# Kernel optimization log

Hardware: AMD Instinct MI355X
Metric: run time of the kernel (lower is better)

## Reference

```python
import jax, jax.numpy as jnp
import numpy as np

N_NODES = 100000


def gcn_conv(x, edge_index, W, b):
    # PyG GCNConv: add self-loops, symmetric normalization, then scatter-add.
    n = x.shape[0]
    loops = jnp.arange(n, dtype=edge_index.dtype)
    src = jnp.concatenate([edge_index[0], loops])
    dst = jnp.concatenate([edge_index[1], loops])
    h = x @ W  # [N, F_out] -- transform before propagate (small GEMM)
    ones = jnp.ones(src.shape[0], dtype=x.dtype)
    deg = jax.ops.segment_sum(ones, dst, num_segments=n)  # in-degree incl. self-loop
    dinv = jnp.where(deg > 0, jax.lax.rsqrt(deg), 0.0)
    norm = dinv[src] * dinv[dst]  # [E+N]
    msg = h[src] * norm[:, None]  # gather + scale, [E+N, F_out]
    out = jax.ops.segment_sum(msg, dst, num_segments=n)  # scatter-add
    return out + b


def setup_inputs() -> dict:
    key = jax.random.key(0)
    k1, k2, k3, k4 = jax.random.split(key, 4)
    d = 128
    x = jax.random.normal(k1, (N_NODES, d), dtype=jnp.float32)
    edge_index = jax.random.randint(k2, (2, 1600000), 0, N_NODES, dtype=jnp.int64)
    scale = 1.0 / np.sqrt(d)
    W1 = jax.random.normal(k3, (d, d), dtype=jnp.float32) * scale
    b1 = jnp.zeros((d,), dtype=jnp.float32)
    W2 = jax.random.normal(k4, (d, d), dtype=jnp.float32) * scale
    b2 = jnp.zeros((d,), dtype=jnp.float32)
    return {"x": x, "edge_index": edge_index, "W1": W1, "b1": b1, "W2": W2, "b2": b2}


def reference(x, edge_index, W1, b1, W2, b2):
    # Layer 1: GCNConv -> relu -> dropout(eval: identity)
    h = jax.nn.relu(gcn_conv(x, edge_index, W1, b1))
    # Layer 2
    h = jax.nn.relu(gcn_conv(h, edge_index, W2, b2))
    return h
```

## Files before the change

### kernel.cpp

```cpp
#include <hip/hip_runtime.h>


#define NFEAT 128
#define BSH 7
#define MAXNB 1024
#define BCAP 4096
#define BPITCH 136

typedef __attribute__((ext_vector_type(8))) short s8v;
typedef __attribute__((ext_vector_type(4))) float f4v;

__device__ inline ushort f2bf(float f) {
    union { float f; uint u; } x; x.f = f;
    uint u = x.u;
    return (ushort)((u + 0x7fffu + ((u >> 16) & 1u)) >> 16);
}
__device__ inline float bf16lo(uint u) { union { uint u; float f; } x; x.u = u << 16; return x.f; }
__device__ inline float bf16hi(uint u) { union { uint u; float f; } x; x.u = u & 0xffff0000u; return x.f; }

__device__ inline void upadd(uint4 v, float* a) {
    a[0] += bf16lo(v.x); a[1] += bf16hi(v.x);
    a[2] += bf16lo(v.y); a[3] += bf16hi(v.y);
    a[4] += bf16lo(v.z); a[5] += bf16hi(v.z);
    a[6] += bf16lo(v.w); a[7] += bf16hi(v.w);
}

__global__ __launch_bounds__(256) void k_bscatter(const int* __restrict__ src,
                                                  const int* __restrict__ dst,
                                                  int* __restrict__ gcnt,
                                                  uint* __restrict__ ebuf,
                                                  int E, int NB, int CH) {
    __shared__ int h[MAXNB];
    int t = threadIdx.x;
    for (int i = t; i < NB; i += 256) h[i] = 0;
    __syncthreads();
    int e0 = blockIdx.x * CH;
    int e1 = min(e0 + CH, E);
    for (int e = e0 + t; e < e1; e += 256) atomicAdd(&h[dst[e] >> BSH], 1);
    __syncthreads();
    for (int i = t; i < NB; i += 256) {
        int c = h[i];
        h[i] = c ? (i * BCAP + atomicAdd(&gcnt[i], c)) : 0;
    }
    __syncthreads();
    for (int e = e0 + t; e < e1; e += 256) {
        int d = dst[e];
        int b = d >> BSH;
        int p = atomicAdd(&h[b], 1);
        if (p < (b + 1) * BCAP)
            ebuf[p] = ((uint)src[e] << BSH) | (uint)(d & ((1 << BSH) - 1));
    }
}

__global__ __launch_bounds__(256) void k_fill2(const uint* __restrict__ ebuf,
                                               const int* __restrict__ gcnt,
                                               int* __restrict__ row_ptr,
                                               float* __restrict__ dinv,
                                               int* __restrict__ col,
                                               int N, int E, int NB) {
    __shared__ int cnt[128];
    __shared__ int pre[128];
    __shared__ int sred[256];
    __shared__ int colL[BCAP];
    int b = blockIdx.x;
    int t = threadIdx.x;
    int part = 0;
    for (int j = t; j < b; j += 256) part += gcnt[j];
    sred[t] = part;
    __syncthreads();
    for (int off = 128; off >= 1; off >>= 1) {
        if (t < off) sred[t] += sred[t + off];
        __syncthreads();
    }
    int gb = sred[0];
    int m = min(gcnt[b], BCAP);
    if (t < 128) cnt[t] = 0;
    __syncthreads();
    const uint* eb = ebuf + (size_t)b * BCAP;
    for (int i = t; i < m; i += 256) atomicAdd(&cnt[eb[i] & 127], 1);
    __syncthreads();
    if (t < 128) pre[t] = cnt[t];
    __syncthreads();
    for (int off = 1; off < 128; off <<= 1) {
        int add = (t >= off && t < 128) ? pre[t - off] : 0;
        __syncthreads();
        if (t < 128) pre[t] += add;
        __syncthreads();
    }
    if (t < 128) {
        pre[t] -= cnt[t];
        int node = (b << BSH) + t;
        if (node < N) {
            row_ptr[node] = gb + pre[t];
            dinv[node] = rsqrtf((float)(cnt[t] + 1));
        }
    }
    __syncthreads();
    for (int i = t; i < m; i += 256) {
        uint p = eb[i];
        int pos = atomicAdd(&pre[p & 127], 1);
        colL[pos] = (int)(p >> BSH);
    }
    __syncthreads();
    for (int i = t; i < m; i += 256) col[gb + i] = colL[i];
    if (b == NB - 1 && t == 0) row_ptr[N] = E;
}

template <bool ABF16>
__global__ __launch_bounds__(256) void k_gemm3(const void* __restrict__ Ap,
                                               const float* __restrict__ W,
                                               const float* __restrict__ dinv,
                                               ushort* __restrict__ hs, int M) {
    __shared__ ushort Bs[128 * BPITCH];
    int t = threadIdx.x;

#pragma unroll
    for (int i = 0; i < 16; i++) {
        int idx = t + i * 256;
        int k4 = idx >> 7;
        int n = idx & 127;
        ushort o[4];
#pragma unroll
        for (int j = 0; j < 4; j++) o[j] = f2bf(W[(k4 * 4 + j) * NFEAT + n]);
        uint2 pk;
        __builtin_memcpy(&pk, o, 8);
        *(uint2*)&Bs[n * BPITCH + k4 * 4] = pk;
    }
    __syncthreads();

    int w = t >> 6, l = t & 63;
    int q = l >> 4, ln = l & 15;
    int wid = blockIdx.x * 4 + w;
    int row0 = wid * 32;
    bool alive = row0 < M;
    if (!alive) row0 = (M - 32) & ~31;

    s8v afr[2][4];
#pragma unroll
    for (int mt = 0; mt < 2; mt++) {
        int row = row0 + mt * 16 + ln;
        if (row >= M) row = M - 1;
        if (ABF16) {
            const ushort* A = (const ushort*)Ap + (size_t)row * NFEAT + q * 8;
#pragma unroll
            for (int ks = 0; ks < 4; ks++)
                afr[mt][ks] = *(const s8v*)(A + ks * 32);
        } else {
            const float* A = (const float*)Ap + (size_t)row * NFEAT + q * 8;
#pragma unroll
            for (int ks = 0; ks < 4; ks++) {
                float4 f0 = *(const float4*)(A + ks * 32);
                float4 f1 = *(const float4*)(A + ks * 32 + 4);
                ushort o[8] = {f2bf(f0.x), f2bf(f0.y), f2bf(f0.z), f2bf(f0.w),
                               f2bf(f1.x), f2bf(f1.y), f2bf(f1.z), f2bf(f1.w)};
                __builtin_memcpy(&afr[mt][ks], o, 16);
            }
        }
    }

    f4v acc[2][8];
#pragma unroll
    for (int mt = 0; mt < 2; mt++)
#pragma unroll
        for (int nt = 0; nt < 8; nt++) acc[mt][nt] = (f4v){0.f, 0.f, 0.f, 0.f};
#pragma unroll
    for (int nt = 0; nt < 8; nt++) {
        const ushort* Bp = Bs + (nt * 16 + ln) * BPITCH + q * 8;
#pragma unroll
        for (int ks = 0; ks < 4; ks++) {
            s8v bfr = *(const s8v*)(Bp + ks * 32);
            acc[0][nt] = __builtin_amdgcn_mfma_f32_16x16x32_bf16(afr[0][ks], bfr, acc[0][nt], 0, 0, 0);
            acc[1][nt] = __builtin_amdgcn_mfma_f32_16x16x32_bf16(afr[1][ks], bfr, acc[1][nt], 0, 0, 0);
        }
    }
    __syncthreads();

    ushort* ow = Bs + w * 32 * NFEAT;
#pragma unroll
    for (int mt = 0; mt < 2; mt++) {
#pragma unroll
        for (int r = 0; r < 4; r++) {
            int lrow = mt * 16 + q * 4 + r;
            float d = dinv[row0 + lrow];
#pragma unroll
            for (int nt = 0; nt < 8; nt++)
                ow[lrow * NFEAT + nt * 16 + ln] = f2bf(acc[mt][nt][r] * d);
        }
    }
    __builtin_amdgcn_s_waitcnt(0);
#pragma unroll
    for (int i = 0; i < 8; i++) {
        int idx = l + i * 64;
        int r = idx >> 4, c = idx & 15;
        uint4 v = *(uint4*)(ow + r * NFEAT + c * 8);
        if (alive) *(uint4*)(hs + (size_t)(row0 + r) * NFEAT + c * 8) = v;
    }
}

template <bool OUT_BF16>
__global__ __launch_bounds__(256) void k_aggregate(const uint4* __restrict__ hs4,
                                                   const int* __restrict__ row_ptr,
                                                   const int* __restrict__ col,
                                                   const float* __restrict__ dinv,
                                                   const float* __restrict__ bias,
                                                   void* __restrict__ outp, int N) {
    int i = blockIdx.x * 4 + (threadIdx.x >> 6);
    if (i >= N) return;
    int lane = threadIdx.x & 63;
    int g = lane >> 4, sub = lane & 15;
    float a[8];
#pragma unroll
    for (int j = 0; j < 8; j++) a[j] = 0.f;
    if (g == 0) upadd(hs4[(size_t)i * 16 + sub], a);
    int s = row_ptr[i], e = row_ptr[i + 1];
    int k = s;
    for (; k + 16 <= e; k += 16) {
        int c0 = col[k + g];
        int c1 = col[k + 4 + g];
        int c2 = col[k + 8 + g];
        int c3 = col[k + 12 + g];
        uint4 v0 = hs4[(size_t)c0 * 16 + sub];
        uint4 v1 = hs4[(size_t)c1 * 16 + sub];
        uint4 v2 = hs4[(size_t)c2 * 16 + sub];
        uint4 v3 = hs4[(size_t)c3 * 16 + sub];
        upadd(v0, a); upadd(v1, a); upadd(v2, a); upadd(v3, a);
    }
    for (; k < e; k += 4) {
        int idx = k + g;
        int c = N;
        if (idx < e) c = col[idx];
        upadd(hs4[(size_t)c * 16 + sub], a);
    }
#pragma unroll
    for (int j = 0; j < 8; j++) {
        a[j] += __shfl_xor(a[j], 16, 64);
        a[j] += __shfl_xor(a[j], 32, 64);
    }
    if (lane < 16) {
        float di = dinv[i];
        const float4* b4 = (const float4*)bias;
        float4 b0 = b4[sub * 2], b1 = b4[sub * 2 + 1];
        float r[8];
        r[0] = fmaxf(fmaf(di, a[0], b0.x), 0.f);
        r[1] = fmaxf(fmaf(di, a[1], b0.y), 0.f);
        r[2] = fmaxf(fmaf(di, a[2], b0.z), 0.f);
        r[3] = fmaxf(fmaf(di, a[3], b0.w), 0.f);
        r[4] = fmaxf(fmaf(di, a[4], b1.x), 0.f);
        r[5] = fmaxf(fmaf(di, a[5], b1.y), 0.f);
        r[6] = fmaxf(fmaf(di, a[6], b1.z), 0.f);
        r[7] = fmaxf(fmaf(di, a[7], b1.w), 0.f);
        if (OUT_BF16) {
            ushort o[8];
#pragma unroll
            for (int j = 0; j < 8; j++) o[j] = f2bf(r[j]);
            uint4 pk;
            __builtin_memcpy(&pk, o, 16);
            ((uint4*)outp)[(size_t)i * 16 + sub] = pk;
        } else {
            float* orow = (float*)outp + (size_t)i * NFEAT + sub * 8;
            *(float4*)orow = make_float4(r[0], r[1], r[2], r[3]);
            *(float4*)(orow + 4) = make_float4(r[4], r[5], r[6], r[7]);
        }
    }
}

extern "C" void kernel_launch(void* const* d_in, const int* in_sizes, int n_in,
                              void* d_out, int out_size, void* d_ws, size_t ws_size,
                              hipStream_t stream) {
    const float* x = (const float*)d_in[0];
    const int* ei = (const int*)d_in[1];
    const float* W1 = (const float*)d_in[2];
    const float* b1 = (const float*)d_in[3];
    const float* W2 = (const float*)d_in[4];
    const float* b2 = (const float*)d_in[5];
    float* out = (float*)d_out;

    const int N = in_sizes[0] / NFEAT;
    const int E = in_sizes[1] / 2;
    const int* src = ei;
    const int* dst = ei + E;
    const int NB = (N + (1 << BSH) - 1) >> BSH;

    char* w = (char*)d_ws;
    size_t off = 0;
    auto alloc = [&](size_t bytes) -> void* {
        void* p = w + off;
        off = (off + bytes + 511) & ~(size_t)511;
        return p;
    };
    ushort* hs = (ushort*)alloc((size_t)(N + 1) * NFEAT * 2);
    ushort* y1 = (ushort*)alloc((size_t)N * NFEAT * 2);
    int* row_ptr = (int*)alloc((size_t)(N + 1) * 4);
    float* dinv = (float*)alloc((size_t)N * 4);
    int* col = (int*)alloc((size_t)E * 4);
    uint* ebuf = (uint*)alloc((size_t)NB * BCAP * 4);
    int* gcnt = (int*)alloc((size_t)MAXNB * 4);
    (void)ws_size; (void)n_in; (void)out_size;

    const int CH = 8192;
    const int chBlk = (E + CH - 1) / CH;

    hipMemsetAsync(gcnt, 0, (size_t)MAXNB * 4, stream);
    hipMemsetAsync(hs + (size_t)N * NFEAT, 0, NFEAT * 2, stream);
    k_bscatter<<<chBlk, 256, 0, stream>>>(src, dst, gcnt, ebuf, E, NB, CH);
    k_fill2<<<NB, 256, 0, stream>>>(ebuf, gcnt, row_ptr, dinv, col, N, E, NB);

    const int gemmBlk = (N + 127) / 128;
    const int aggBlk = (N + 3) / 4;

    k_gemm3<false><<<gemmBlk, 256, 0, stream>>>(x, W1, dinv, hs, N);
    k_aggregate<true><<<aggBlk, 256, 0, stream>>>((const uint4*)hs, row_ptr, col, dinv, b1, y1, N);
    k_gemm3<true><<<gemmBlk, 256, 0, stream>>>(y1, W2, dinv, hs, N);
    k_aggregate<false><<<aggBlk, 256, 0, stream>>>((const uint4*)hs, row_ptr, col, dinv, b2, out, N);
}
```

Before: 316.5 us.

## Pack aggregation accumulators as float2, shrink scatter chunk, drop zero-row memset

```diff
diff --git a/kernel.cpp b/kernel.cpp
--- a/kernel.cpp
+++ b/kernel.cpp
@@ -9,6 +9,7 @@
 
 typedef __attribute__((ext_vector_type(8))) short s8v;
 typedef __attribute__((ext_vector_type(4))) float f4v;
+typedef __attribute__((ext_vector_type(2))) float f2v;
 
 __device__ inline ushort f2bf(float f) {
     union { float f; uint u; } x; x.f = f;
@@ -17,12 +18,17 @@
 }
 __device__ inline float bf16lo(uint u) { union { uint u; float f; } x; x.u = u << 16; return x.f; }
 __device__ inline float bf16hi(uint u) { union { uint u; float f; } x; x.u = u & 0xffff0000u; return x.f; }
-
-__device__ inline void upadd(uint4 v, float* a) {
-    a[0] += bf16lo(v.x); a[1] += bf16hi(v.x);
-    a[2] += bf16lo(v.y); a[3] += bf16hi(v.y);
-    a[4] += bf16lo(v.z); a[5] += bf16hi(v.z);
-    a[6] += bf16lo(v.w); a[7] += bf16hi(v.w);
+__device__ inline f2v unpk(uint u) {
+    union { uint u; float f; } lo, hi;
+    lo.u = u << 16;
+    hi.u = u & 0xffff0000u;
+    return (f2v){lo.f, hi.f};
+}
+__device__ inline void upadd2(uint4 v, f2v* a) {
+    a[0] += unpk(v.x);
+    a[1] += unpk(v.y);
+    a[2] += unpk(v.z);
+    a[3] += unpk(v.w);
 }
 
 __global__ __launch_bounds__(256) void k_bscatter(const int* __restrict__ src,
@@ -113,6 +119,7 @@
                                                ushort* __restrict__ hs, int M) {
     __shared__ ushort Bs[128 * BPITCH];
     int t = threadIdx.x;
+    if (blockIdx.x == 0 && t < 64) ((uint*)(hs + (size_t)M * NFEAT))[t] = 0;
 
 #pragma unroll
     for (int i = 0; i < 16; i++) {
@@ -208,10 +215,10 @@
     if (i >= N) return;
     int lane = threadIdx.x & 63;
     int g = lane >> 4, sub = lane & 15;
-    float a[8];
-#pragma unroll
-    for (int j = 0; j < 8; j++) a[j] = 0.f;
-    if (g == 0) upadd(hs4[(size_t)i * 16 + sub], a);
+    f2v a[4];
+#pragma unroll
+    for (int j = 0; j < 4; j++) a[j] = (f2v){0.f, 0.f};
+    if (g == 0) upadd2(hs4[(size_t)i * 16 + sub], a);
     int s = row_ptr[i], e = row_ptr[i + 1];
     int k = s;
     for (; k + 16 <= e; k += 16) {
@@ -223,32 +230,34 @@
         uint4 v1 = hs4[(size_t)c1 * 16 + sub];
         uint4 v2 = hs4[(size_t)c2 * 16 + sub];
         uint4 v3 = hs4[(size_t)c3 * 16 + sub];
-        upadd(v0, a); upadd(v1, a); upadd(v2, a); upadd(v3, a);
+        upadd2(v0, a); upadd2(v1, a); upadd2(v2, a); upadd2(v3, a);
     }
     for (; k < e; k += 4) {
         int idx = k + g;
         int c = N;
         if (idx < e) c = col[idx];
-        upadd(hs4[(size_t)c * 16 + sub], a);
-    }
-#pragma unroll
-    for (int j = 0; j < 8; j++) {
-        a[j] += __shfl_xor(a[j], 16, 64);
-        a[j] += __shfl_xor(a[j], 32, 64);
+        upadd2(hs4[(size_t)c * 16 + sub], a);
+    }
+#pragma unroll
+    for (int j = 0; j < 4; j++) {
+        a[j].x += __shfl_xor(a[j].x, 16, 64);
+        a[j].y += __shfl_xor(a[j].y, 16, 64);
+        a[j].x += __shfl_xor(a[j].x, 32, 64);
+        a[j].y += __shfl_xor(a[j].y, 32, 64);
     }
     if (lane < 16) {
         float di = dinv[i];
         const float4* b4 = (const float4*)bias;
         float4 b0 = b4[sub * 2], b1 = b4[sub * 2 + 1];
         float r[8];
-        r[0] = fmaxf(fmaf(di, a[0], b0.x), 0.f);
-        r[1] = fmaxf(fmaf(di, a[1], b0.y), 0.f);
-        r[2] = fmaxf(fmaf(di, a[2], b0.z), 0.f);
-        r[3] = fmaxf(fmaf(di, a[3], b0.w), 0.f);
-        r[4] = fmaxf(fmaf(di, a[4], b1.x), 0.f);
-        r[5] = fmaxf(fmaf(di, a[5], b1.y), 0.f);
-        r[6] = fmaxf(fmaf(di, a[6], b1.z), 0.f);
-        r[7] = fmaxf(fmaf(di, a[7], b1.w), 0.f);
+        r[0] = fmaxf(fmaf(di, a[0].x, b0.x), 0.f);
+        r[1] = fmaxf(fmaf(di, a[0].y, b0.y), 0.f);
+        r[2] = fmaxf(fmaf(di, a[1].x, b0.z), 0.f);
+        r[3] = fmaxf(fmaf(di, a[1].y, b0.w), 0.f);
+        r[4] = fmaxf(fmaf(di, a[2].x, b1.x), 0.f);
+        r[5] = fmaxf(fmaf(di, a[2].y, b1.y), 0.f);
+        r[6] = fmaxf(fmaf(di, a[3].x, b1.z), 0.f);
+        r[7] = fmaxf(fmaf(di, a[3].y, b1.w), 0.f);
         if (OUT_BF16) {
             ushort o[8];
 #pragma unroll
@@ -297,11 +306,10 @@
     int* gcnt = (int*)alloc((size_t)MAXNB * 4);
     (void)ws_size; (void)n_in; (void)out_size;
 
-    const int CH = 8192;
+    const int CH = 2048;
     const int chBlk = (E + CH - 1) / CH;
 
     hipMemsetAsync(gcnt, 0, (size_t)MAXNB * 4, stream);
-    hipMemsetAsync(hs + (size_t)N * NFEAT, 0, NFEAT * 2, stream);
     k_bscatter<<<chBlk, 256, 0, stream>>>(src, dst, gcnt, ebuf, E, NB, CH);
     k_fill2<<<NB, 256, 0, stream>>>(ebuf, gcnt, row_ptr, dinv, col, N, E, NB);
 
```

New measurement: 314.6 us. About the same (-0.6%).
